# Optimization experiments

Measured on AMD Instinct MI355X. Metric: run time of the kernel, lower is better.

Reference implementation:

```python
import jax, jax.numpy as jnp
import numpy as np

B, T, D = 32, 512, 768
K, H = 256, 512


def setup_inputs() -> dict:
    key = jax.random.key(0)
    ks = jax.random.split(key, 5)
    s = 0.02  # keep pre-activations in a sane range
    return {
        "inputs": jax.random.normal(ks[0], (B, T, D), jnp.float32),
        "W_x": jax.random.normal(ks[1], (K + 1, 4 * H), jnp.float32) * s,
        "W_h": jax.random.normal(ks[2], (H, 4 * H), jnp.float32) * s,
        "b_lstm": jnp.zeros((4 * H,), jnp.float32),
        "W_key": jax.random.normal(ks[3], (H, K), jnp.float32) * s,
        "b_key": jnp.zeros((K,), jnp.float32),
        "W_g": jax.random.normal(ks[4], (H, 1), jnp.float32) * s,
        "b_g": jnp.zeros((1,), jnp.float32),
        "conf_gain": jnp.ones((), jnp.float32),
        "conf_bias": jnp.zeros((), jnp.float32),
    }


def reference(inputs, W_x, W_h, b_lstm, W_key, b_key, W_g, b_g, conf_gain, conf_bias):
    Bq, Tq, Dq = inputs.shape
    Kq = W_key.shape[1]
    Hq = W_h.shape[0]
    t_idx = jnp.arange(Tq)
    xs = jnp.transpose(inputs, (1, 0, 2))  # [T, B, D]

    def step(carry, xt):
        t, x = xt  # t: scalar step index, x: [B, D]
        key_r, h, c, M_k, M_v = carry
        # Keras LSTMCell (gate order i, f, c, o); input is previous key_r [B, K+1]
        z = key_r @ W_x + h @ W_h + b_lstm
        i, f, g_c, o = jnp.split(z, 4, axis=-1)
        i = jax.nn.sigmoid(i)
        f = jax.nn.sigmoid(f)
        g_c = jnp.tanh(g_c)
        o = jax.nn.sigmoid(o)
        c = f * c + i * g_c
        h = o * jnp.tanh(c)  # lstm_out == hidden in Keras LSTMCell
        key_w = h @ W_key + b_key            # [B, K]
        g = jax.nn.sigmoid(h @ W_g + b_g)    # [B, 1]
        # similarity attention over all previously written memory slots
        sim = jnp.einsum('bd,tbd->bt', x, M_v)          # [B, T]
        mask = (t_idx < t)[None, :]                     # valid slots only
        w_k = jax.nn.softmax(jnp.where(mask, sim, -1e30), axis=1)
        c_k = jax.nn.sigmoid(sim * conf_gain + conf_bias)
        aug = jnp.concatenate([jnp.transpose(M_k, (1, 0, 2)), c_k[:, :, None]], axis=2)  # [B, T, K+1]
        key_r_new = jnp.where(t > 0, g * jnp.einsum('bt,btk->bk', w_k, aug), 0.0)
        M_k = M_k.at[t].set(key_w)
        M_v = M_v.at[t].set(x)
        return (key_r_new, h, c, M_k, M_v), None

    init = (
        jnp.zeros((Bq, Kq + 1), inputs.dtype),
        jnp.zeros((Bq, Hq), inputs.dtype),
        jnp.zeros((Bq, Hq), inputs.dtype),
        jnp.zeros((Tq, Bq, Kq), inputs.dtype),
        jnp.zeros((Tq, Bq, Dq), inputs.dtype),
    )
    (key_r, h, c, M_k, M_v), _ = jax.lax.scan(step, init, (t_idx, xs))
    return h  # final lstm_out
```

## Files before the change

kernel.cpp:

```cpp
#include <hip/hip_runtime.h>
#include <math.h>

#define BQ 32
#define TQ 512
#define DQ 768
#define KQ 256
#define HQ 512
#define G4 2048
#define SROW 772
#define NWG 512
#define NTHR 256
#define NBG 4

typedef float f32x4 __attribute__((ext_vector_type(4)));

__device__ __forceinline__ void waitcnt0() {
  asm volatile("s_waitcnt vmcnt(0) lgkmcnt(0)" ::: "memory");
}
__device__ __forceinline__ void st_dev(float* p, float v) {
  asm volatile("global_store_dword %0, %1, off sc1" :: "v"(p), "v"(v) : "memory");
}
__device__ __forceinline__ int ld_flag(const int* p) {
  int v;
  asm volatile("global_load_dword %0, %1, off sc1\ns_waitcnt vmcnt(0)"
               : "=v"(v) : "v"(p) : "memory");
  return v;
}
__device__ __forceinline__ void wg_wait(const int* flags, int target) {
  if (threadIdx.x < 64) {
    for (;;) {
      int v = ld_flag(flags + threadIdx.x);
      if (__all(v >= target)) break;
      __builtin_amdgcn_s_sleep(2);
    }
  }
  __syncthreads();
}
__device__ __forceinline__ void wg_signal(int* flag, int val) {
  waitcnt0();
  __syncthreads();
  if (threadIdx.x == 0)
    asm volatile("global_store_dword %0, %1, off sc1" :: "v"(flag), "v"(val) : "memory");
}
__device__ __forceinline__ float sigm(float x) { return 1.f / (1.f + __expf(-x)); }

__global__ void __launch_bounds__(256) gram_k(const float* __restrict__ X,
                                              float* __restrict__ Gm) {
  __shared__ __align__(16) float As[64 * 33];
  __shared__ __align__(16) float Bs[64 * 33];
  const int bid = blockIdx.x;
  const int b = blockIdx.y;
  int I = 0, base = 0;
  while (base + I + 1 <= bid) { base += I + 1; ++I; }
  const int J = bid - base;
  const int t0 = I * 64, u0 = J * 64;
  const float* Xb = X + (size_t)b * TQ * DQ;
  const int ty = threadIdx.x >> 4, tx = threadIdx.x & 15;
  const int sc = threadIdx.x & 31, sr = threadIdx.x >> 5;
  float acc[4][4];
#pragma unroll
  for (int i = 0; i < 4; ++i)
#pragma unroll
    for (int j = 0; j < 4; ++j) acc[i][j] = 0.f;
  for (int k0 = 0; k0 < DQ; k0 += 32) {
#pragma unroll
    for (int rr = 0; rr < 8; ++rr) {
      const int r = rr * 8 + sr;
      As[r * 33 + sc] = Xb[(size_t)(t0 + r) * DQ + k0 + sc];
      Bs[r * 33 + sc] = Xb[(size_t)(u0 + r) * DQ + k0 + sc];
    }
    __syncthreads();
#pragma unroll
    for (int k = 0; k < 32; ++k) {
      float av[4], bv[4];
#pragma unroll
      for (int i = 0; i < 4; ++i) av[i] = As[(ty * 4 + i) * 33 + k];
#pragma unroll
      for (int j = 0; j < 4; ++j) bv[j] = Bs[(tx * 4 + j) * 33 + k];
#pragma unroll
      for (int i = 0; i < 4; ++i)
#pragma unroll
        for (int j = 0; j < 4; ++j) acc[i][j] += av[i] * bv[j];
    }
    __syncthreads();
  }
  float* gb = Gm + (size_t)b * TQ * TQ;
#pragma unroll
  for (int i = 0; i < 4; ++i) {
    f32x4 o;
    o.x = acc[i][0]; o.y = acc[i][1]; o.z = acc[i][2]; o.w = acc[i][3];
    *(f32x4*)&gb[(size_t)(t0 + ty * 4 + i) * TQ + u0 + tx * 4] = o;
  }
}

__global__ void __launch_bounds__(256) smax_k(float* __restrict__ Gm,
                                              float* __restrict__ Sv,
                                              const float* __restrict__ cgp,
                                              const float* __restrict__ cbp) {
  const int t = blockIdx.x + 1;
  const int b = blockIdx.y;
  const int tid = threadIdx.x;
  const int lane = tid & 63;
  const int wv = tid >> 6;
  __shared__ float row[TQ];
  __shared__ float r1[4], r2[4], r3[4];
  float* R = Gm + ((size_t)b * TQ + t) * TQ;
  const float cg = cgp[0], cb = cbp[0];
  for (int i = tid; i < t; i += 256) row[i] = R[i];
  __syncthreads();
  float m = -3e38f;
  for (int i = tid; i < t; i += 256) m = fmaxf(m, row[i]);
#pragma unroll
  for (int k = 1; k < 64; k <<= 1) m = fmaxf(m, __shfl_xor(m, k));
  if (lane == 0) r1[wv] = m;
  __syncthreads();
  m = fmaxf(fmaxf(r1[0], r1[1]), fmaxf(r1[2], r1[3]));
  float s = 0.f, sck = 0.f;
  for (int i = tid; i < t; i += 256) {
    const float r = row[i];
    const float e = __expf(r - m);
    const float ck = 1.f / (1.f + __expf(-(r * cg + cb)));
    row[i] = e; s += e; sck += e * ck;
  }
#pragma unroll
  for (int k = 1; k < 64; k <<= 1) { s += __shfl_xor(s, k); sck += __shfl_xor(sck, k); }
  if (lane == 0) { r2[wv] = s; r3[wv] = sck; }
  __syncthreads();
  s = r2[0] + r2[1] + r2[2] + r2[3];
  sck = r3[0] + r3[1] + r3[2] + r3[3];
  const float inv = 1.f / s;
  for (int i = tid; i < t; i += 256) R[i] = row[i] * inv;
  if (tid == 0) Sv[(size_t)b * TQ + t] = sck * inv;
}

__global__ void __launch_bounds__(NTHR, 2) esbn_scan(
    const float* __restrict__ Wx, const float* __restrict__ Wh,
    const float* __restrict__ bl, const float* __restrict__ Wk,
    const float* __restrict__ bk, const float* __restrict__ Wg,
    const float* __restrict__ bgp, const float* __restrict__ Wmat,
    const float* __restrict__ Sv, float* buf, int* flagsX, int* flagsY,
    float* __restrict__ out) {
  (void)flagsY;
  __shared__ __align__(16) float st[NBG * SROW];
  __shared__ __align__(16) float wrow[NBG * TQ];
  __shared__ __align__(16) float Mk_s[16 * 520];
  __shared__ __align__(16) float wkey_s[4 * 520];
  __shared__ float wgv[HQ];
  __shared__ __align__(16) float zred[4 * 8 * 4 * 4];
  __shared__ float c_s[NBG * 8];
  __shared__ float gg_s[NBG];
  __shared__ float bl_s[32];
  __shared__ float bk_s[4];
  __shared__ float bg_s;

  const int tid = threadIdx.x;
  const int wg = blockIdx.x & 63;
  const int grp = blockIdx.x >> 6;
  const int b0 = grp * NBG;
  const int dc = tid >> 3;
  const int cg = tid & 7;

  int colg[4];
#pragma unroll
  for (int j = 0; j < 4; ++j) {
    const int c = cg * 4 + j;
    colg[j] = (c >> 3) * HQ + wg * 8 + (c & 7);
  }
  f32x4 wh[16], wxr[8], wxl;
#pragma unroll
  for (int i = 0; i < 16; ++i) {
    const int d = (i << 5) + dc;
    wh[i].x = Wh[(size_t)d * G4 + colg[0]];
    wh[i].y = Wh[(size_t)d * G4 + colg[1]];
    wh[i].z = Wh[(size_t)d * G4 + colg[2]];
    wh[i].w = Wh[(size_t)d * G4 + colg[3]];
  }
#pragma unroll
  for (int i = 0; i < 8; ++i) {
    const int d = (i << 5) + dc;
    wxr[i].x = Wx[(size_t)d * G4 + colg[0]];
    wxr[i].y = Wx[(size_t)d * G4 + colg[1]];
    wxr[i].z = Wx[(size_t)d * G4 + colg[2]];
    wxr[i].w = Wx[(size_t)d * G4 + colg[3]];
  }
  wxl.x = wxl.y = wxl.z = wxl.w = 0.f;
  if (dc == 0) {
    wxl.x = Wx[(size_t)256 * G4 + colg[0]];
    wxl.y = Wx[(size_t)256 * G4 + colg[1]];
    wxl.z = Wx[(size_t)256 * G4 + colg[2]];
    wxl.w = Wx[(size_t)256 * G4 + colg[3]];
  }
  for (int i = tid; i < NBG * SROW; i += NTHR) st[i] = 0.f;
  for (int i = tid; i < 16 * 520; i += NTHR) Mk_s[i] = 0.f;
  for (int i = tid; i < 4 * 520; i += NTHR) {
    const int kl = i / 520, u = i - kl * 520;
    wkey_s[i] = (u < HQ) ? Wk[(size_t)u * KQ + wg * 4 + kl] : 0.f;
  }
  for (int i = tid; i < HQ; i += NTHR) wgv[i] = Wg[i];
  if (tid < 32) bl_s[tid] = bl[(tid >> 3) * HQ + wg * 8 + (tid & 7)];
  if (tid < 4) bk_s[tid] = bk[wg * 4 + tid];
  if (tid == 0) bg_s = bgp[0];
  if (tid < NBG * 8) c_s[tid] = 0.f;
  __syncthreads();

  int* f = flagsX + grp * 64;
  const int yb = tid >> 6;
  const int ykl = (tid >> 4) & 3;
  const int ytc = tid & 15;
  const int lt = tid & 63;

  const int i0 = tid, i1 = tid + 256, i2 = tid + 512;
  const int sb0 = i0 / 192, so0 = i0 - sb0 * 192;
  const int sb1 = i1 / 192, so1 = i1 - sb1 * 192;
  const int sb2 = i2 / 192, so2 = i2 - sb2 * 192;
  const int sj0 = sb0 * SROW + ((so0 < 128) ? (so0 << 2) : (512 + ((so0 - 128) << 2)));
  const int sj1 = sb1 * SROW + ((so1 < 128) ? (so1 << 2) : (512 + ((so1 - 128) << 2)));
  const int sj2 = sb2 * SROW + ((so2 < 128) ? (so2 << 2) : (512 + ((so2 - 128) << 2)));

  for (int t = 0; t < TQ; ++t) {
    const int p = t & 1, pn = p ^ 1;
    float wv8[8];
    const bool rowv = (t >= 1) && (t < TQ - 1);
    if (rowv) {
      const float* wr = Wmat + ((size_t)(b0 + yb) * TQ + t) * TQ + lt;
#pragma unroll
      for (int k = 0; k < 8; ++k) wv8[k] = wr[k << 6];
    }
    if (t > 0) {
      wg_wait(f, t);
      float* base = buf + (size_t)(p * BQ + b0) * SROW;
      f32x4 v0, v1, v2;
      const float* q0 = base + sj0;
      const float* q1 = base + sj1;
      const float* q2 = base + sj2;
      asm volatile("global_load_dwordx4 %0, %1, off sc1" : "=v"(v0) : "v"(q0));
      asm volatile("global_load_dwordx4 %0, %1, off sc1" : "=v"(v1) : "v"(q1));
      asm volatile("global_load_dwordx4 %0, %1, off sc1" : "=v"(v2) : "v"(q2));
      float sv = 0.f;
      if (tid < 4) sv = Sv[(size_t)(b0 + tid) * TQ + (t - 1)];
      asm volatile("s_waitcnt vmcnt(0)" : "+v"(v0), "+v"(v1), "+v"(v2) : : "memory");
      *(f32x4*)&st[sj0] = v0;
      *(f32x4*)&st[sj1] = v1;
      *(f32x4*)&st[sj2] = v2;
      if (tid < 4) st[tid * SROW + 768] = sv;
    }
    __syncthreads();
    {
      float a = 0.f;
#pragma unroll
      for (int k = 0; k < 8; ++k) {
        const int u = lt + (k << 6);
        a += st[yb * SROW + u] * wgv[u];
      }
#pragma unroll
      for (int m = 1; m <= 32; m <<= 1) a += __shfl_xor(a, m);
      if (lt == 0) gg_s[yb] = sigm(a + bg_s);
    }
    f32x4 acc[NBG], pk[NBG];
#pragma unroll
    for (int b = 0; b < NBG; ++b) {
      acc[b].x = acc[b].y = acc[b].z = acc[b].w = 0.f;
      pk[b].x = pk[b].y = pk[b].z = pk[b].w = 0.f;
    }
#pragma unroll
    for (int i = 0; i < 16; ++i) {
      const f32x4 w = wh[i];
      const int d = (i << 5) + dc;
#pragma unroll
      for (int b = 0; b < NBG; ++b) acc[b] += st[b * SROW + d] * w;
    }
#pragma unroll
    for (int i = 0; i < 8; ++i) {
      const f32x4 w = wxr[i];
      const int d = 512 + (i << 5) + dc;
#pragma unroll
      for (int b = 0; b < NBG; ++b) pk[b] += st[b * SROW + d] * w;
    }
    if (dc == 0) {
#pragma unroll
      for (int b = 0; b < NBG; ++b) pk[b] += st[b * SROW + 768] * wxl;
    }
    __syncthreads();
#pragma unroll
    for (int b = 0; b < NBG; ++b) {
      const float g = gg_s[b];
      acc[b].x += g * pk[b].x; acc[b].y += g * pk[b].y;
      acc[b].z += g * pk[b].z; acc[b].w += g * pk[b].w;
    }
#pragma unroll
    for (int m = 8; m <= 32; m <<= 1) {
#pragma unroll
      for (int b = 0; b < NBG; ++b) {
        acc[b].x += __shfl_xor(acc[b].x, m);
        acc[b].y += __shfl_xor(acc[b].y, m);
        acc[b].z += __shfl_xor(acc[b].z, m);
        acc[b].w += __shfl_xor(acc[b].w, m);
      }
    }
    if (lt < 8) {
      const int wv = tid >> 6;
#pragma unroll
      for (int b = 0; b < NBG; ++b)
        *(f32x4*)&zred[((wv * 8 + lt) * 4 + b) * 4] = acc[b];
    }
    __syncthreads();
    if (tid < 32) {
      const int b = tid >> 3, u = tid & 7;
      float zg[4];
#pragma unroll
      for (int g = 0; g < 4; ++g) {
        const int cgi = g * 2 + (u >> 2), comp = u & 3;
        float z = bl_s[g * 8 + u];
#pragma unroll
        for (int wv = 0; wv < 4; ++wv) z += zred[((wv * 8 + cgi) * 4 + b) * 4 + comp];
        zg[g] = z;
      }
      const float gi = sigm(zg[0]);
      const float gf = sigm(zg[1]);
      const float go = sigm(zg[3]);
      const float cn = gf * c_s[tid] + gi * tanhf(zg[2]);
      const float hv = go * tanhf(cn);
      c_s[tid] = cn;
      if (t == TQ - 1) out[(size_t)(b0 + b) * HQ + wg * 8 + u] = hv;
      else st_dev(buf + (size_t)(pn * BQ + b0 + b) * SROW + wg * 8 + u, hv);
    }
    if (t == TQ - 1) break;
    if (t >= 1) {
#pragma unroll
      for (int k = 0; k < 8; ++k) wrow[yb * TQ + lt + (k << 6)] = wv8[k];
      float kw = 0.f;
      const float* hrow = &st[yb * SROW];
      const float* wkr = &wkey_s[ykl * 520];
#pragma unroll
      for (int j = 0; j < 32; ++j) {
        const int u = ytc + (j << 4);
        kw += hrow[u] * wkr[u];
      }
      kw += __shfl_xor(kw, 1);
      kw += __shfl_xor(kw, 2);
      kw += __shfl_xor(kw, 4);
      kw += __shfl_xor(kw, 8);
      if (ytc == 0) Mk_s[(yb * 4 + ykl) * 520 + (t - 1)] = kw + bk_s[ykl];
      float accA = 0.f;
      const float* mk = &Mk_s[(yb * 4 + ykl) * 520];
      const float* wb = &wrow[yb * TQ];
#pragma unroll
      for (int j = 0; j < 32; ++j) {
        const int u = ytc + (j << 4);
        accA += wb[u] * mk[u];
      }
      accA += __shfl_xor(accA, 1);
      accA += __shfl_xor(accA, 2);
      accA += __shfl_xor(accA, 4);
      accA += __shfl_xor(accA, 8);
      if (ytc == 0)
        st_dev(buf + (size_t)(pn * BQ + b0 + yb) * SROW + 512 + wg * 4 + ykl, accA);
    }
    wg_signal(&f[wg], t + 1);
  }
}

extern "C" void kernel_launch(void* const* d_in, const int* in_sizes, int n_in,
                              void* d_out, int out_size, void* d_ws, size_t ws_size,
                              hipStream_t stream) {
  (void)in_sizes; (void)n_in; (void)out_size; (void)ws_size;
  const float* X  = (const float*)d_in[0];
  const float* Wx = (const float*)d_in[1];
  const float* Wh = (const float*)d_in[2];
  const float* bl = (const float*)d_in[3];
  const float* Wk = (const float*)d_in[4];
  const float* bk = (const float*)d_in[5];
  const float* Wg = (const float*)d_in[6];
  const float* bg = (const float*)d_in[7];
  const float* cg = (const float*)d_in[8];
  const float* cb = (const float*)d_in[9];
  float* out = (float*)d_out;
  float* ws = (float*)d_ws;

  float* Gm = ws;
  float* Sv = ws + (size_t)8388608;
  float* buf = ws + (size_t)8404992;
  int* flagsX = (int*)(ws + (size_t)8454400);
  int* flagsY = flagsX + 512;

  hipMemsetAsync(Sv, 0, (size_t)(16384 + 49408 + 1024) * 4, stream);
  gram_k<<<dim3(36, BQ), dim3(256), 0, stream>>>(X, Gm);
  smax_k<<<dim3(TQ - 1, BQ), dim3(256), 0, stream>>>(Gm, Sv, cg, cb);

  void* args[] = {(void*)&Wx, (void*)&Wh, (void*)&bl, (void*)&Wk, (void*)&bk,
                  (void*)&Wg, (void*)&bg, (void*)&Gm, (void*)&Sv,
                  (void*)&buf, (void*)&flagsX, (void*)&flagsY, (void*)&out};
  hipError_t e = hipLaunchCooperativeKernel((const void*)esbn_scan, dim3(NWG),
                                            dim3(NTHR), args, 0, stream);
  if (e != hipSuccess) {
    esbn_scan<<<dim3(NWG), dim3(NTHR), 0, stream>>>(Wx, Wh, bl, Wk, bk, Wg, bg,
                                                    Gm, Sv, buf, flagsX,
                                                    flagsY, out);
  }
}
```

Baseline: 4.686 ms.

## Replace per-workgroup flag polling with atomic counter barrier and preload confidence sums

Swaps the 64-flag polling barrier for a single atomic counter per batch group that each workgroup increments and waiters poll until it reaches 64*t. The Sv confidence values are preloaded into shared memory once instead of being fetched from global memory every step. The gate reduction is computed redundantly per wave in registers, which removes one __syncthreads per step. The risk is contention on the atomic counter across 64 workgroups each step, traded for cheaper polling.

After: 4.646 ms. No clear change (-0.9%).

```diff
diff --git a/kernel.cpp b/kernel.cpp
--- a/kernel.cpp
+++ b/kernel.cpp
@@ -7,7 +7,8 @@
 #define KQ 256
 #define HQ 512
 #define G4 2048
-#define SROW 772
+#define BROW 768
+#define STP 772
 #define NWG 512
 #define NTHR 256
 #define NBG 4
@@ -20,27 +21,22 @@
 __device__ __forceinline__ void st_dev(float* p, float v) {
   asm volatile("global_store_dword %0, %1, off sc1" :: "v"(p), "v"(v) : "memory");
 }
-__device__ __forceinline__ int ld_flag(const int* p) {
+__device__ __forceinline__ int ld_dev(const int* p) {
   int v;
   asm volatile("global_load_dword %0, %1, off sc1\ns_waitcnt vmcnt(0)"
                : "=v"(v) : "v"(p) : "memory");
   return v;
 }
-__device__ __forceinline__ void wg_wait(const int* flags, int target) {
+__device__ __forceinline__ void wg_wait_ctr(const int* ctr, int target) {
   if (threadIdx.x < 64) {
-    for (;;) {
-      int v = ld_flag(flags + threadIdx.x);
-      if (__all(v >= target)) break;
-      __builtin_amdgcn_s_sleep(2);
-    }
-  }
-  __syncthreads();
-}
-__device__ __forceinline__ void wg_signal(int* flag, int val) {
+    while (ld_dev(ctr) < target) __builtin_amdgcn_s_sleep(1);
+  }
+  __syncthreads();
+}
+__device__ __forceinline__ void wg_signal_ctr(int* ctr) {
   waitcnt0();
   __syncthreads();
-  if (threadIdx.x == 0)
-    asm volatile("global_store_dword %0, %1, off sc1" :: "v"(flag), "v"(val) : "memory");
+  if (threadIdx.x == 0) atomicAdd(ctr, 1);
 }
 __device__ __forceinline__ float sigm(float x) { return 1.f / (1.f + __expf(-x)); }
 
@@ -138,17 +134,16 @@
     const float* __restrict__ bl, const float* __restrict__ Wk,
     const float* __restrict__ bk, const float* __restrict__ Wg,
     const float* __restrict__ bgp, const float* __restrict__ Wmat,
-    const float* __restrict__ Sv, float* buf, int* flagsX, int* flagsY,
+    const float* __restrict__ Sv, float* buf, int* ctrs,
     float* __restrict__ out) {
-  (void)flagsY;
-  __shared__ __align__(16) float st[NBG * SROW];
+  __shared__ __align__(16) float st[NBG * STP];
   __shared__ __align__(16) float wrow[NBG * TQ];
   __shared__ __align__(16) float Mk_s[16 * 520];
   __shared__ __align__(16) float wkey_s[4 * 520];
-  __shared__ float wgv[HQ];
+  __shared__ __align__(16) float wgv[HQ];
+  __shared__ __align__(16) float svl[NBG * TQ];
   __shared__ __align__(16) float zred[4 * 8 * 4 * 4];
   __shared__ float c_s[NBG * 8];
-  __shared__ float gg_s[NBG];
   __shared__ float bl_s[32];
   __shared__ float bk_s[4];
   __shared__ float bg_s;
@@ -190,32 +185,35 @@
     wxl.z = Wx[(size_t)256 * G4 + colg[2]];
     wxl.w = Wx[(size_t)256 * G4 + colg[3]];
   }
-  for (int i = tid; i < NBG * SROW; i += NTHR) st[i] = 0.f;
+  for (int i = tid; i < NBG * STP; i += NTHR) st[i] = 0.f;
   for (int i = tid; i < 16 * 520; i += NTHR) Mk_s[i] = 0.f;
   for (int i = tid; i < 4 * 520; i += NTHR) {
     const int kl = i / 520, u = i - kl * 520;
     wkey_s[i] = (u < HQ) ? Wk[(size_t)u * KQ + wg * 4 + kl] : 0.f;
   }
   for (int i = tid; i < HQ; i += NTHR) wgv[i] = Wg[i];
+  for (int i = tid; i < NBG * TQ; i += NTHR)
+    svl[i] = Sv[(size_t)(b0 + (i >> 9)) * TQ + (i & 511)];
   if (tid < 32) bl_s[tid] = bl[(tid >> 3) * HQ + wg * 8 + (tid & 7)];
   if (tid < 4) bk_s[tid] = bk[wg * 4 + tid];
   if (tid == 0) bg_s = bgp[0];
   if (tid < NBG * 8) c_s[tid] = 0.f;
   __syncthreads();
 
-  int* f = flagsX + grp * 64;
+  int* ctr = ctrs + grp * 32;
   const int yb = tid >> 6;
   const int ykl = (tid >> 4) & 3;
   const int ytc = tid & 15;
   const int lt = tid & 63;
 
-  const int i0 = tid, i1 = tid + 256, i2 = tid + 512;
-  const int sb0 = i0 / 192, so0 = i0 - sb0 * 192;
-  const int sb1 = i1 / 192, so1 = i1 - sb1 * 192;
-  const int sb2 = i2 / 192, so2 = i2 - sb2 * 192;
-  const int sj0 = sb0 * SROW + ((so0 < 128) ? (so0 << 2) : (512 + ((so0 - 128) << 2)));
-  const int sj1 = sb1 * SROW + ((so1 < 128) ? (so1 << 2) : (512 + ((so1 - 128) << 2)));
-  const int sj2 = sb2 * SROW + ((so2 < 128) ? (so2 << 2) : (512 + ((so2 - 128) << 2)));
+  int sgo[3], slo[3];
+#pragma unroll
+  for (int k = 0; k < 3; ++k) {
+    const int c = tid + (k << 8);
+    const int b = c / 192, off = (c - b * 192) << 2;
+    sgo[k] = (b << 9) + (b << 8) + off;
+    slo[k] = b * STP + off;
+  }
 
   for (int t = 0; t < TQ; ++t) {
     const int p = t & 1, pn = p ^ 1;
@@ -227,34 +225,39 @@
       for (int k = 0; k < 8; ++k) wv8[k] = wr[k << 6];
     }
     if (t > 0) {
-      wg_wait(f, t);
-      float* base = buf + (size_t)(p * BQ + b0) * SROW;
+      wg_wait_ctr(ctr, 64 * t);
+      const float* base = buf + (size_t)(p * BQ + b0) * BROW;
       f32x4 v0, v1, v2;
-      const float* q0 = base + sj0;
-      const float* q1 = base + sj1;
-      const float* q2 = base + sj2;
+      const float* q0 = base + sgo[0];
+      const float* q1 = base + sgo[1];
+      const float* q2 = base + sgo[2];
       asm volatile("global_load_dwordx4 %0, %1, off sc1" : "=v"(v0) : "v"(q0));
       asm volatile("global_load_dwordx4 %0, %1, off sc1" : "=v"(v1) : "v"(q1));
       asm volatile("global_load_dwordx4 %0, %1, off sc1" : "=v"(v2) : "v"(q2));
-      float sv = 0.f;
-      if (tid < 4) sv = Sv[(size_t)(b0 + tid) * TQ + (t - 1)];
       asm volatile("s_waitcnt vmcnt(0)" : "+v"(v0), "+v"(v1), "+v"(v2) : : "memory");
-      *(f32x4*)&st[sj0] = v0;
-      *(f32x4*)&st[sj1] = v1;
-      *(f32x4*)&st[sj2] = v2;
-      if (tid < 4) st[tid * SROW + 768] = sv;
+      *(f32x4*)&st[slo[0]] = v0;
+      *(f32x4*)&st[slo[1]] = v1;
+      *(f32x4*)&st[slo[2]] = v2;
     }
     __syncthreads();
+    float gv[NBG];
     {
+      const int sb = lt >> 4, sl = lt & 15;
       float a = 0.f;
-#pragma unroll
-      for (int k = 0; k < 8; ++k) {
-        const int u = lt + (k << 6);
-        a += st[yb * SROW + u] * wgv[u];
+      const float* hb = &st[sb * STP + (sl << 2)];
+      const float* wb = &wgv[sl << 2];
+#pragma unroll
+      for (int j = 0; j < 8; ++j) {
+        const f32x4 hv = *(const f32x4*)&hb[j << 6];
+        const f32x4 wv = *(const f32x4*)&wb[j << 6];
+        a += hv.x * wv.x + hv.y * wv.y + hv.z * wv.z + hv.w * wv.w;
       }
-#pragma unroll
-      for (int m = 1; m <= 32; m <<= 1) a += __shfl_xor(a, m);
-      if (lt == 0) gg_s[yb] = sigm(a + bg_s);
+      a += __shfl_xor(a, 1);
+      a += __shfl_xor(a, 2);
+      a += __shfl_xor(a, 4);
+      a += __shfl_xor(a, 8);
+#pragma unroll
+      for (int b = 0; b < NBG; ++b) gv[b] = sigm(__shfl(a, b << 4) + bg_s);
     }
     f32x4 acc[NBG], pk[NBG];
 #pragma unroll
@@ -267,23 +270,22 @@
       const f32x4 w = wh[i];
       const int d = (i << 5) + dc;
 #pragma unroll
-      for (int b = 0; b < NBG; ++b) acc[b] += st[b * SROW + d] * w;
+      for (int b = 0; b < NBG; ++b) acc[b] += st[b * STP + d] * w;
     }
 #pragma unroll
     for (int i = 0; i < 8; ++i) {
       const f32x4 w = wxr[i];
       const int d = 512 + (i << 5) + dc;
 #pragma unroll
-      for (int b = 0; b < NBG; ++b) pk[b] += st[b * SROW + d] * w;
-    }
-    if (dc == 0) {
-#pragma unroll
-      for (int b = 0; b < NBG; ++b) pk[b] += st[b * SROW + 768] * wxl;
-    }
-    __syncthreads();
+      for (int b = 0; b < NBG; ++b) pk[b] += st[b * STP + d] * w;
+    }
+    if (dc == 0 && t > 0) {
+#pragma unroll
+      for (int b = 0; b < NBG; ++b) pk[b] += svl[(b << 9) + t - 1] * wxl;
+    }
 #pragma unroll
     for (int b = 0; b < NBG; ++b) {
-      const float g = gg_s[b];
+      const float g = gv[b];
       acc[b].x += g * pk[b].x; acc[b].y += g * pk[b].y;
       acc[b].z += g * pk[b].z; acc[b].w += g * pk[b].w;
     }
@@ -322,14 +324,14 @@
       const float hv = go * tanhf(cn);
       c_s[tid] = cn;
       if (t == TQ - 1) out[(size_t)(b0 + b) * HQ + wg * 8 + u] = hv;
-      else st_dev(buf + (size_t)(pn * BQ + b0 + b) * SROW + wg * 8 + u, hv);
+      else st_dev(buf + (size_t)(pn * BQ + b0 + b) * BROW + wg * 8 + u, hv);
     }
     if (t == TQ - 1) break;
     if (t >= 1) {
 #pragma unroll
       for (int k = 0; k < 8; ++k) wrow[yb * TQ + lt + (k << 6)] = wv8[k];
       float kw = 0.f;
-      const float* hrow = &st[yb * SROW];
+      const float* hrow = &st[yb * STP];
       const float* wkr = &wkey_s[ykl * 520];
 #pragma unroll
       for (int j = 0; j < 32; ++j) {
@@ -354,9 +356,9 @@
       accA += __shfl_xor(accA, 4);
       accA += __shfl_xor(accA, 8);
       if (ytc == 0)
-        st_dev(buf + (size_t)(pn * BQ + b0 + yb) * SROW + 512 + wg * 4 + ykl, accA);
-    }
-    wg_signal(&f[wg], t + 1);
+        st_dev(buf + (size_t)(pn * BQ + b0 + yb) * BROW + 512 + wg * 4 + ykl, accA);
+    }
+    wg_signal_ctr(ctr);
   }
 }
 
@@ -380,21 +382,19 @@
   float* Gm = ws;
   float* Sv = ws + (size_t)8388608;
   float* buf = ws + (size_t)8404992;
-  int* flagsX = (int*)(ws + (size_t)8454400);
-  int* flagsY = flagsX + 512;
-
-  hipMemsetAsync(Sv, 0, (size_t)(16384 + 49408 + 1024) * 4, stream);
+  int* ctrs = (int*)(ws + (size_t)8454144);
+
+  hipMemsetAsync(Sv, 0, (size_t)(16384 + 49152 + 256) * 4, stream);
   gram_k<<<dim3(36, BQ), dim3(256), 0, stream>>>(X, Gm);
   smax_k<<<dim3(TQ - 1, BQ), dim3(256), 0, stream>>>(Gm, Sv, cg, cb);
 
   void* args[] = {(void*)&Wx, (void*)&Wh, (void*)&bl, (void*)&Wk, (void*)&bk,
                   (void*)&Wg, (void*)&bg, (void*)&Gm, (void*)&Sv,
-                  (void*)&buf, (void*)&flagsX, (void*)&flagsY, (void*)&out};
+                  (void*)&buf, (void*)&ctrs, (void*)&out};
   hipError_t e = hipLaunchCooperativeKernel((const void*)esbn_scan, dim3(NWG),
                                             dim3(NTHR), args, 0, stream);
   if (e != hipSuccess) {
     esbn_scan<<<dim3(NWG), dim3(NTHR), 0, stream>>>(Wx, Wh, bl, Wk, bk, Wg, bg,
-                                                    Gm, Sv, buf, flagsX,
-                                                    flagsY, out);
-  }
-}
+                                                    Gm, Sv, buf, ctrs, out);
+  }
+}
```
